# Performance work log

Measured on AMD Instinct MI355X. Metric: run time of the kernel, lower is better.

The kernel has to match this reference:

```python
import jax, jax.numpy as jnp
import numpy as np

D = 256      # input_dim
H = 8        # n_heads
HD = D // H  # head_dim = 32
B = 8
S = 127      # seq_len (feature tokens)
N = S + 1    # new_seq (CLS + features)
LN_EPS = 1e-5


def setup_inputs() -> dict:
    key = jax.random.key(0)
    ks = jax.random.split(key, 20)
    g = 0.02
    inp = {
        "desc_embeddings": jax.random.normal(ks[0], (B, S, D), jnp.float32),
        "name_value_embeddings": jax.random.normal(ks[1], (B, N, D), jnp.float32),
        # q/k/v projections (stored [in, out])
        "wq": jax.random.normal(ks[2], (D, D), jnp.float32) * g,
        "bq": jnp.zeros((D,), jnp.float32),
        "wk": jax.random.normal(ks[3], (D, D), jnp.float32) * g,
        "bk": jnp.zeros((D,), jnp.float32),
        "wv": jax.random.normal(ks[4], (D, D), jnp.float32) * g,
        "bv": jnp.zeros((D,), jnp.float32),
        # edge_update: Linear(2D->D), LayerNorm(D), ReLU, Linear(D->D)
        "ew1": jax.random.normal(ks[5], (2 * D, D), jnp.float32) * g,
        "eb1": jnp.zeros((D,), jnp.float32),
        "ln_g": jnp.ones((D,), jnp.float32),
        "ln_b": jnp.zeros((D,), jnp.float32),
        "ew2": jax.random.normal(ks[6], (D, D), jnp.float32) * g,
        "eb2": jnp.zeros((D,), jnp.float32),
        # attn_proj: Linear(3*head_dim -> 1)
        "attn_w": jax.random.normal(ks[7], (3 * HD,), jnp.float32) * g,
        "attn_b": jnp.zeros((), jnp.float32),
        # out_proj
        "wo": jax.random.normal(ks[8], (D, D), jnp.float32) * g,
        "bo": jnp.zeros((D,), jnp.float32),
    }
    return inp


def _forward(desc, nv, wq, bq, wk, bk, wv, bv, ew1, eb1, ln_g, ln_b, ew2, eb2,
             attn_w, attn_b, wo, bo):
    b, n, d = nv.shape
    s = n - 1
    # new adjacency: [1:,1:] = ones minus diag; row 0 (CLS->var) = 1; col 0 = 0; [0,0]=0
    adj = jnp.zeros((n, n), nv.dtype)
    adj = adj.at[1:, 1:].set(1.0 - jnp.eye(s, dtype=nv.dtype))
    adj = adj.at[0, 1:].set(1.0)
    adj = jnp.broadcast_to(adj, (b, n, n))  # [B,N,N]

    # edge attributes: var-var pairs concat(desc_i, desc_j); CLS row/col concat(desc_j, desc_j)
    var_edge = jnp.concatenate([
        jnp.broadcast_to(desc[:, :, None, :], (b, s, s, d)),
        jnp.broadcast_to(desc[:, None, :, :], (b, s, s, d)),
    ], axis=-1)                                   # [B,S,S,2D]
    cls_edge = jnp.concatenate([desc, desc], -1)  # [B,S,2D]
    ea = jnp.zeros((b, n, n, 2 * d), nv.dtype)
    ea = ea.at[:, 1:, 1:, :].set(var_edge)
    ea = ea.at[:, 0, 1:, :].set(cls_edge)
    ea = ea.at[:, 1:, 0, :].set(cls_edge)

    # edge MLP: Linear -> LayerNorm -> ReLU -> Linear
    h = ea @ ew1 + eb1                            # [B,N,N,D]
    mu = jnp.mean(h, -1, keepdims=True)
    var = jnp.mean((h - mu) ** 2, -1, keepdims=True)
    h = (h - mu) * jax.lax.rsqrt(var + LN_EPS) * ln_g + ln_b
    h = jax.nn.relu(h)
    e = h @ ew2 + eb2                             # [B,N,N,D]
    e = e.reshape(b, n, n, H, HD).transpose(0, 3, 1, 2, 4)  # [B,H,N,N,hd]
    e = e * adj[:, None, :, :, None]

    def heads(x, w, bias):
        return (x @ w + bias).reshape(b, n, H, HD).transpose(0, 2, 1, 3)  # [B,H,N,hd]

    q = heads(nv, wq, bq)
    k = heads(nv, wk, bk)
    v = heads(nv, wv, bv)

    # attn_proj(cat(q_i, k_j, e_ij)) decomposes additively over the three chunks
    w_q, w_k, w_e = attn_w[:HD], attn_w[HD:2 * HD], attn_w[2 * HD:]
    aq = jnp.einsum('bhid,d->bhi', q, w_q)
    ak = jnp.einsum('bhjd,d->bhj', k, w_k)
    ae = jnp.einsum('bhijd,d->bhij', e, w_e)
    scores = aq[:, :, :, None] + ak[:, :, None, :] + ae + attn_b  # [B,H,N,N]
    scores = scores + (adj[:, None] == 0).astype(scores.dtype) * (-1e9)
    attn = jax.nn.softmax(scores, axis=-1)

    ctx = jnp.einsum('bhij,bhjd->bhid', attn, v)                  # [B,H,N,hd]
    ctx = ctx.transpose(0, 2, 1, 3).reshape(b, n, d)
    out = ctx @ wo + bo
    return out, attn


def reference(desc_embeddings, name_value_embeddings, wq, bq, wk, bk, wv, bv,
              ew1, eb1, ln_g, ln_b, ew2, eb2, attn_w, attn_b, wo, bo):
    return _forward(desc_embeddings, name_value_embeddings, wq, bq, wk, bk, wv, bv,
                    ew1, eb1, ln_g, ln_b, ew2, eb2, attn_w, attn_b, wo, bo)
```

## Files before the change

kernel.cpp:

```cpp
#include <hip/hip_runtime.h>
#include <math.h>

namespace {
constexpr int D = 256;
constexpr int H = 8;
constexpr int HD = 32;
constexpr int B = 8;
constexpr int S = 127;
constexpr int N = 128;
constexpr float LN_EPS = 1e-5f;

constexpr int WS_P1T = 0;
constexpr int WS_P2T = WS_P1T + B * D * N;
constexpr int WS_V   = WS_P2T + B * D * N;
constexpr int WS_AQ  = WS_V + B * N * D;
constexpr int WS_AK  = WS_AQ + B * H * N;
constexpr int WS_FQK = WS_AK + B * H * N;
constexpr int WS_V2  = WS_FQK + D * 16;
constexpr int WS_BF  = WS_V2 + D * H;
constexpr int WS_ST  = WS_BF + 32;
constexpr int WS_RSTD = WS_ST + B * 512;
constexpr int WS_MB   = WS_RSTD + B * N * N;

typedef float f32x2 __attribute__((ext_vector_type(2)));
union F4 { float4 v; f32x2 h[2]; float f[4]; };
}

__global__ __launch_bounds__(256) void k1_fold(
    const float* __restrict__ wq, const float* __restrict__ wk,
    const float* __restrict__ ew2, const float* __restrict__ bq,
    const float* __restrict__ bk, const float* __restrict__ eb2,
    const float* __restrict__ attn_w, float* __restrict__ ws) {
  float* FQK = ws + WS_FQK;
  float* V2T = ws + WS_V2;
  float* BF  = ws + WS_BF;
  const int tg = blockIdx.x * 256 + threadIdx.x;
  if (tg < 6144) {
    const int mat = tg >> 11;
    const int rem = tg & 2047;
    const int c = rem >> 3;
    const int h = rem & 7;
    const float* W = (mat == 0) ? wq : (mat == 1) ? wk : ew2;
    const float* aw = attn_w + mat * HD;
    const float* wrow = W + c * D + h * HD;
    float s = 0.f;
#pragma unroll
    for (int d = 0; d < HD; ++d) s = fmaf(wrow[d], aw[d], s);
    if (mat < 2) FQK[c * 16 + mat * 8 + h] = s;
    else         V2T[h * D + c] = s;
  } else if (tg < 6168) {
    const int idx = tg - 6144;
    const int mat = idx >> 3;
    const int h = idx & 7;
    const float* bias = (mat == 0) ? bq : (mat == 1) ? bk : eb2;
    const float* aw = attn_w + mat * HD;
    float s = 0.f;
#pragma unroll
    for (int d = 0; d < HD; ++d) s = fmaf(bias[h * HD + d], aw[d], s);
    BF[mat * 8 + h] = s;
  }
}

__global__ __launch_bounds__(256) void kA_pre(
    const float* __restrict__ desc, const float* __restrict__ ew1,
    const float* __restrict__ eb1,
    const float* __restrict__ nv, const float* __restrict__ wv,
    const float* __restrict__ bv, float* __restrict__ ws) {
  const int blk = blockIdx.x;
  const int t = threadIdx.x;
  __shared__ float rows[4][264];
  __shared__ float fqks[D * 16];
  __shared__ float aqred2[2][64];

  if (blk < 256) {
    float* P1Tf = ws + WS_P1T;
    float* P2Tf = ws + WS_P2T;
    const int b = blk >> 5;
    const int i0 = (blk & 31) * 4;
    {
      const int r = t >> 6, c4 = t & 63;
      const int row = i0 + r;
      F4 dv;
      if (row < S) dv.v = *(const float4*)&desc[(b * S + row) * D + c4 * 4];
      else         dv.v = make_float4(0.f, 0.f, 0.f, 0.f);
      *(float4*)&rows[r][c4 * 4] = dv.v;
    }
    __syncthreads();
    const int o4 = t & 63;
    const int grp = t >> 6;
    const int m = grp >> 1;
    const int rp = grp & 1;
    const float* W = ew1 + m * D * D;
    F4 a0, a1;
    a0.v = make_float4(0.f, 0.f, 0.f, 0.f);
    a1.v = make_float4(0.f, 0.f, 0.f, 0.f);
    for (int c2 = 0; c2 < D; ++c2) {
      F4 w; w.v = *(const float4*)&W[c2 * D + o4 * 4];
      const float s0 = rows[rp * 2][c2];
      const float s1 = rows[rp * 2 + 1][c2];
#pragma unroll
      for (int e = 0; e < 4; ++e) {
        a0.f[e] = fmaf(s0, w.f[e], a0.f[e]);
        a1.f[e] = fmaf(s1, w.f[e], a1.f[e]);
      }
    }
    F4 ebv;
    if (m == 0) ebv.v = *(const float4*)&eb1[o4 * 4];
    else        ebv.v = make_float4(0.f, 0.f, 0.f, 0.f);
    F4 o0, o1;
#pragma unroll
    for (int e = 0; e < 4; ++e) {
      o0.f[e] = a0.f[e] + ebv.f[e];
      o1.f[e] = a1.f[e] + ebv.f[e];
    }
    float* PT = (m == 0) ? P1Tf : P2Tf;
    const int rbase = (b * 64 + o4) * 512;
    const int row0i = i0 + rp * 2;
    const int row1i = row0i + 1;
    if (row0i < S) *(float4*)&PT[rbase + row0i * 4] = o0.v;
    if (row1i < S) *(float4*)&PT[rbase + row1i * 4] = o1.v;
    float sv0 = 0.f, qv0 = 0.f, sv1 = 0.f, qv1 = 0.f;
#pragma unroll
    for (int e = 0; e < 4; ++e) {
      sv0 += o0.f[e]; qv0 = fmaf(o0.f[e], o0.f[e], qv0);
      sv1 += o1.f[e]; qv1 = fmaf(o1.f[e], o1.f[e], qv1);
    }
#pragma unroll
    for (int o = 1; o < 64; o <<= 1) {
      sv0 += __shfl_xor(sv0, o);
      qv0 += __shfl_xor(qv0, o);
      sv1 += __shfl_xor(sv1, o);
      qv1 += __shfl_xor(qv1, o);
    }
    if (o4 == 0) {
      float* STW = ws + WS_ST + b * 512 + m * 256;
      if (row0i < S) { STW[row0i] = sv0; STW[128 + row0i] = qv0; }
      if (row1i < S) { STW[row1i] = sv1; STW[128 + row1i] = qv1; }
    }
  } else {
    float* Vf  = ws + WS_V;
    float* AQ  = ws + WS_AQ;
    float* AK  = ws + WS_AK;
    const float* FQK = ws + WS_FQK;
    const float* BF  = ws + WS_BF;
    const int blk2 = blk - 256;
    const int b = blk2 >> 5;
    const int j0 = (blk2 & 31) * 4;
    {
      const int r = t >> 6, c4 = t & 63;
      *(float4*)&rows[r][c4 * 4] =
          *(const float4*)&nv[(b * N + j0 + r) * D + c4 * 4];
      float4* fq4 = (float4*)fqks;
      const float4* FQK4 = (const float4*)FQK;
#pragma unroll
      for (int k = 0; k < 4; ++k) fq4[k * 256 + t] = FQK4[k * 256 + t];
    }
    __syncthreads();
    if (t < 64) {
      const int o4 = t;
      F4 acc[4];
#pragma unroll
      for (int r = 0; r < 4; ++r) acc[r].v = make_float4(0.f, 0.f, 0.f, 0.f);
      for (int c2 = 0; c2 < D; ++c2) {
        F4 w; w.v = *(const float4*)&wv[c2 * D + o4 * 4];
#pragma unroll
        for (int r = 0; r < 4; ++r) {
          const float s = rows[r][c2];
#pragma unroll
          for (int e = 0; e < 4; ++e)
            acc[r].f[e] = fmaf(s, w.f[e], acc[r].f[e]);
        }
      }
      F4 b4; b4.v = *(const float4*)&bv[o4 * 4];
#pragma unroll
      for (int r = 0; r < 4; ++r) {
#pragma unroll
        for (int e = 0; e < 4; ++e) acc[r].f[e] += b4.f[e];
        *(float4*)&Vf[(b * N + j0 + r) * D + o4 * 4] = acc[r].v;
      }
    } else if (t < 192) {
      const int idx = t - 64;
      const int il = idx >> 5;
      const int oi = idx & 15;
      const int ch = (idx >> 4) & 1;
      float s = 0.f;
      for (int c = ch * 128; c < ch * 128 + 128; ++c)
        s = fmaf(rows[il][c], fqks[c * 16 + oi], s);
      aqred2[ch][il * 16 + oi] = s;
    }
    __syncthreads();
    if (t < 64) {
      const int il = t >> 4, oi = t & 15;
      const float s2 = aqred2[0][t] + aqred2[1][t] + BF[oi];
      if (oi < 8) AQ[(b * H + oi) * N + j0 + il] = s2;
      else        AK[(b * H + (oi - 8)) * N + j0 + il] = s2;
    }
  }
}

__global__ __launch_bounds__(512) void kG_stats(float* __restrict__ ws) {
  const int bid = blockIdx.x;
  const int wg = (bid & 7) * 32 + (bid >> 3);
  const int b = wg >> 5;
  const int ip0 = (wg & 31) * 4;
  const int t = threadIdx.x;
  const int jp = t & 127;
  const int cg = t >> 7;

  __shared__ float p1t[1024];
  __shared__ float gred[4][4][128];

  const float* P1Tf = ws + WS_P1T;
  const float4* P24 = reinterpret_cast<const float4*>(ws + WS_P2T);
  const float* ST = ws + WS_ST + b * 512;
  float* RST = ws + WS_RSTD + b * N * N;
  float* MBP = ws + WS_MB + b * N * N;
  const int base4 = b * 64 * 128;

  for (int k = t; k < 1024; k += 512) {
    const int r = k >> 8, c = k & 255;
    const int row = ip0 + r;
    p1t[r * 256 + c] = (row < S)
        ? P1Tf[(b * 64 + (c >> 2)) * 512 + row * 4 + (c & 3)] : 0.f;
  }
  F4 pp[16];
#pragma unroll
  for (int cc = 0; cc < 16; ++cc)
    pp[cc].v = P24[base4 + (cg * 16 + cc) * 128 + jp];
  __syncthreads();

  float g[4] = {0.f, 0.f, 0.f, 0.f};
#pragma unroll
  for (int cc = 0; cc < 16; ++cc) {
    const int c4 = cg * 16 + cc;
#pragma unroll
    for (int r = 0; r < 4; ++r) {
      F4 p1; p1.v = *(const float4*)&p1t[r * 256 + c4 * 4];
      g[r] = fmaf(pp[cc].f[0], p1.f[0], g[r]);
      g[r] = fmaf(pp[cc].f[1], p1.f[1], g[r]);
      g[r] = fmaf(pp[cc].f[2], p1.f[2], g[r]);
      g[r] = fmaf(pp[cc].f[3], p1.f[3], g[r]);
    }
  }
#pragma unroll
  for (int r = 0; r < 4; ++r) gred[cg][r][jp] = g[r];
  __syncthreads();
  {
    const int r2 = t >> 7, jp2 = t & 127;
    const float G = gred[0][r2][jp2] + gred[1][r2][jp2]
                  + gred[2][r2][jp2] + gred[3][r2][jp2];
    const int ip = ip0 + r2;
    const float S1 = ST[0 * 128 + ip], Q1 = ST[1 * 128 + ip];
    const float S2 = ST[2 * 128 + jp2], Q2 = ST[3 * 128 + jp2];
    const float mean = (S1 + S2) * (1.f / 256.f);
    const float var = (Q1 + Q2 + 2.f * G) * (1.f / 256.f) - mean * mean;
    const float rstd = 1.f / sqrtf(var + LN_EPS);
    RST[ip * N + jp2] = rstd;
    MBP[ip * N + jp2] = -mean * rstd;
  }
}

__global__ __launch_bounds__(512) void k4_attn(
    const float* __restrict__ ws,
    const float* __restrict__ ln_g, const float* __restrict__ ln_b,
    const float* __restrict__ attn_bp, float* __restrict__ attnp) {
  const int bid = blockIdx.x;
  const int wg = (bid & 7) * 64 + (bid >> 3);
  const int b = wg >> 6;
  const int i0 = (wg & 63) * 2;
  const int t = threadIdx.x;
  const int jl = t & 127;
  const int cq = t >> 7;

  __shared__ float v2s[H * D];
  __shared__ float gbs[2 * D];
  __shared__ float p1e[2][D];
  __shared__ float dsh[4][128][9];
  __shared__ float aqs[2][8];
  __shared__ float redm[8][2], reds[8][2];

  const float* P1Tf = ws + WS_P1T;
  const float* AQ   = ws + WS_AQ;
  const float* AK   = ws + WS_AK;
  const float* BF   = ws + WS_BF;
  const float* v2p  = ws + WS_V2;
  const float* RST  = ws + WS_RSTD + b * N * N;
  const float* MBP  = ws + WS_MB + b * N * N;

  reinterpret_cast<float4*>(v2s)[t] = reinterpret_cast<const float4*>(v2p)[t];
  if (t < 256) { gbs[t] = ln_g[t]; gbs[256 + t] = ln_b[t]; }
  {
    const int r = t >> 8, c = t & 255;
    const int row = i0 + r - 1;
    p1e[r][c] = (row >= 0)
        ? P1Tf[(b * 64 + (c >> 2)) * 512 + row * 4 + (c & 3)] : 0.f;
  }
  if (t < 16) {
    const int r = t >> 3, h = t & 7;
    aqs[r][h] = AQ[(b * H + h) * N + i0 + r] + BF[16 + h] + attn_bp[0];
  }

  const int jm1 = (jl == 0) ? 0 : jl - 1;
  const bool blk0 = (i0 == 0);
  f32x2 rstd2[2], mb2[2];
#pragma unroll
  for (int r = 0; r < 2; ++r) {
    const int irow = i0 + r;
    const int ip = (irow == 0) ? jm1 : (irow - 1);
    const float rs = RST[ip * N + jm1];
    const float mb = MBP[ip * N + jm1];
    rstd2[r].x = rs; rstd2[r].y = rs;
    mb2[r].x = mb; mb2[r].y = mb;
  }
  float akr[2];
#pragma unroll
  for (int hh = 0; hh < 2; ++hh)
    akr[hh] = AK[(b * H + cq * 2 + hh) * N + jl];
  const f32x2 zero2 = {0.f, 0.f};
  __syncthreads();

  const float4* P14 = reinterpret_cast<const float4*>(ws + WS_P1T);
  const float4* P24 = reinterpret_cast<const float4*>(ws + WS_P2T);
  const int base4 = b * 64 * 128;
  const int c4lo = cq * 16;

  f32x2 dt2[2][8];
#pragma unroll
  for (int r = 0; r < 2; ++r)
#pragma unroll
    for (int h = 0; h < 8; ++h) dt2[r][h] = zero2;
  F4 p2c;
  p2c.v = P24[base4 + c4lo * 128 + jm1];
  for (int cc = 0; cc < 16; ++cc) {
    const int c4 = c4lo + cc;
    F4 p2 = p2c;
    if (cc < 15) p2c.v = P24[base4 + (c4 + 1) * 128 + jm1];
    F4 g4; g4.v = *(const float4*)&gbs[c4 * 4];
    F4 b4; b4.v = *(const float4*)&gbs[256 + c4 * 4];
    F4 p1r[2];
    if (blk0) p1r[0].v = P14[base4 + c4 * 128 + jm1];
    else      p1r[0].v = *(const float4*)&p1e[0][c4 * 4];
    p1r[1].v = *(const float4*)&p1e[1][c4 * 4];
    f32x2 w2[2][2];
#pragma unroll
    for (int r = 0; r < 2; ++r) {
#pragma unroll
      for (int pp = 0; pp < 2; ++pp) {
        const f32x2 u2 = p1r[r].h[pp] + p2.h[pp];
        const f32x2 zt2 = __builtin_elementwise_fma(u2, rstd2[r], mb2[r]);
        const f32x2 z2 = __builtin_elementwise_fma(zt2, g4.h[pp], b4.h[pp]);
        w2[r][pp] = __builtin_elementwise_max(z2, zero2);
      }
    }
#pragma unroll
    for (int h = 0; h < 8; ++h) {
      F4 v2v; v2v.v = *(const float4*)&v2s[h * D + c4 * 4];
      dt2[0][h] = __builtin_elementwise_fma(w2[0][0], v2v.h[0], dt2[0][h]);
      dt2[0][h] = __builtin_elementwise_fma(w2[0][1], v2v.h[1], dt2[0][h]);
      dt2[1][h] = __builtin_elementwise_fma(w2[1][0], v2v.h[0], dt2[1][h]);
      dt2[1][h] = __builtin_elementwise_fma(w2[1][1], v2v.h[1], dt2[1][h]);
    }
  }

  const int w = t >> 6;
  for (int r = 0; r < 2; ++r) {
#pragma unroll
    for (int h = 0; h < 8; ++h) dsh[cq][jl][h] = dt2[r][h].x + dt2[r][h].y;
    __syncthreads();
    const int irow = i0 + r;
    const bool masked = (jl == 0) || (jl == irow);
    float sc[2], pr[2];
#pragma unroll
    for (int hh = 0; hh < 2; ++hh) {
      const int h = cq * 2 + hh;
      const float dsum = dsh[0][jl][h] + dsh[1][jl][h]
                       + dsh[2][jl][h] + dsh[3][jl][h];
      const float v = aqs[r][h] + akr[hh] + dsum;
      sc[hh] = masked ? -INFINITY : v;
    }
    float mx[2];
#pragma unroll
    for (int hh = 0; hh < 2; ++hh) {
      float v = sc[hh];
#pragma unroll
      for (int o = 1; o < 64; o <<= 1) v = fmaxf(v, __shfl_xor(v, o));
      mx[hh] = v;
    }
    if ((t & 63) == 0) { redm[w][0] = mx[0]; redm[w][1] = mx[1]; }
    __syncthreads();
#pragma unroll
    for (int hh = 0; hh < 2; ++hh) {
      const float m = fmaxf(redm[w][hh], redm[w ^ 1][hh]);
      pr[hh] = expf(sc[hh] - m);
    }
    float sm[2];
#pragma unroll
    for (int hh = 0; hh < 2; ++hh) {
      float v = pr[hh];
#pragma unroll
      for (int o = 1; o < 64; o <<= 1) v += __shfl_xor(v, o);
      sm[hh] = v;
    }
    if ((t & 63) == 0) { reds[w][0] = sm[0]; reds[w][1] = sm[1]; }
    __syncthreads();
#pragma unroll
    for (int hh = 0; hh < 2; ++hh) {
      const int h = cq * 2 + hh;
      const float at = pr[hh] / (reds[w][hh] + reds[w ^ 1][hh]);
      attnp[((b * H + h) * N + irow) * N + jl] = at;
    }
    __syncthreads();
  }
}

__global__ __launch_bounds__(512) void k5_out(
    const float* __restrict__ ws, const float* __restrict__ attnp,
    const float* __restrict__ wo, const float* __restrict__ bo,
    float* __restrict__ outp) {
  const int bid = blockIdx.x;
  const int wg = (bid & 7) * 32 + (bid >> 3);
  const int b = wg >> 5;
  const int i0 = (wg & 31) * 4;
  const int t = threadIdx.x;
  const int o4 = t & 63;
  const int grp = t >> 6;

  __shared__ float attn_sh[4][H][136];
  __shared__ float red[4][8][64][4];
  __shared__ float ctxs[4][260];

#pragma unroll
  for (int k = 0; k < 2; ++k) {
    const int idx = k * 512 + t;
    const int r = idx >> 8, h = (idx >> 5) & 7, j4 = idx & 31;
    const float4 a =
        *(const float4*)&attnp[((b * H + h) * N + i0 + r) * N + j4 * 4];
    *(float4*)&attn_sh[r][h][j4 * 4] = a;
  }
  __syncthreads();

  const int hh = o4 >> 3;
  const float* Vb = ws + WS_V + b * N * D;
  F4 acc[4];
#pragma unroll
  for (int r = 0; r < 4; ++r) acc[r].v = make_float4(0.f, 0.f, 0.f, 0.f);
  for (int jj = 0; jj < 16; ++jj) {
    const int j = grp * 16 + jj;
    F4 v4; v4.v = *(const float4*)&Vb[j * D + o4 * 4];
#pragma unroll
    for (int r = 0; r < 4; ++r) {
      const float a = attn_sh[r][hh][j];
#pragma unroll
      for (int e = 0; e < 4; ++e) acc[r].f[e] = fmaf(a, v4.f[e], acc[r].f[e]);
    }
  }
#pragma unroll
  for (int r = 0; r < 4; ++r) *(float4*)&red[r][grp][o4][0] = acc[r].v;
  __syncthreads();
  if (t < 256) {
    const int oc = t & 63, r = t >> 6;
    F4 s; s.v = make_float4(0.f, 0.f, 0.f, 0.f);
#pragma unroll
    for (int g = 0; g < 8; ++g) {
      F4 p; p.v = *(const float4*)&red[r][g][oc][0];
#pragma unroll
      for (int e = 0; e < 4; ++e) s.f[e] += p.f[e];
    }
    *(float4*)&ctxs[r][oc * 4] = s.v;
  }
  __syncthreads();

  F4 acc2[4];
#pragma unroll
  for (int r = 0; r < 4; ++r) acc2[r].v = make_float4(0.f, 0.f, 0.f, 0.f);
  for (int cc = 0; cc < 32; ++cc) {
    const int c2 = grp * 32 + cc;
    F4 w4; w4.v = *(const float4*)&wo[c2 * D + o4 * 4];
#pragma unroll
    for (int r = 0; r < 4; ++r) {
      const float cx = ctxs[r][c2];
#pragma unroll
      for (int e = 0; e < 4; ++e)
        acc2[r].f[e] = fmaf(cx, w4.f[e], acc2[r].f[e]);
    }
  }
#pragma unroll
  for (int r = 0; r < 4; ++r) *(float4*)&red[r][grp][o4][0] = acc2[r].v;
  __syncthreads();
  if (t < 256) {
    const int oc = t & 63, r = t >> 6;
    F4 s; s.v = *(const float4*)&bo[oc * 4];
#pragma unroll
    for (int g = 0; g < 8; ++g) {
      F4 p; p.v = *(const float4*)&red[r][g][oc][0];
#pragma unroll
      for (int e = 0; e < 4; ++e) s.f[e] += p.f[e];
    }
    *(float4*)&outp[(b * N + i0 + r) * D + oc * 4] = s.v;
  }
}

extern "C" void kernel_launch(void* const* d_in, const int* in_sizes, int n_in,
                              void* d_out, int out_size, void* d_ws, size_t ws_size,
                              hipStream_t stream) {
  (void)in_sizes; (void)n_in; (void)out_size; (void)ws_size;
  const float* desc = (const float*)d_in[0];
  const float* nv   = (const float*)d_in[1];
  const float* wq   = (const float*)d_in[2];
  const float* bq   = (const float*)d_in[3];
  const float* wk   = (const float*)d_in[4];
  const float* bk   = (const float*)d_in[5];
  const float* wv   = (const float*)d_in[6];
  const float* bv   = (const float*)d_in[7];
  const float* ew1  = (const float*)d_in[8];
  const float* eb1  = (const float*)d_in[9];
  const float* ln_g = (const float*)d_in[10];
  const float* ln_b = (const float*)d_in[11];
  const float* ew2  = (const float*)d_in[12];
  const float* eb2  = (const float*)d_in[13];
  const float* aw   = (const float*)d_in[14];
  const float* ab   = (const float*)d_in[15];
  const float* wo   = (const float*)d_in[16];
  const float* bo   = (const float*)d_in[17];

  float* ws   = (float*)d_ws;
  float* outp = (float*)d_out;
  float* attnp = outp + B * N * D;

  k1_fold<<<25, 256, 0, stream>>>(wq, wk, ew2, bq, bk, eb2, aw, ws);
  kA_pre<<<512, 256, 0, stream>>>(desc, ew1, eb1, nv, wv, bv, ws);
  kG_stats<<<256, 512, 0, stream>>>(ws);
  k4_attn<<<B * 64, 512, 0, stream>>>(ws, ln_g, ln_b, ab, attnp);
  k5_out<<<256, 512, 0, stream>>>(ws, attnp, wo, bo, outp);
}
```

Baseline: 52.61 us.

## Widen row tiles in pre-projection and attention kernels, split-K with LDS reduction

kA_pre now runs 512-thread blocks that each handle 8 rows instead of 4. The K dimension is split across four thread groups and the partial sums are combined through a shared-memory reduction, so each weight load is reused across more rows. k4_attn now processes 4 query rows per block instead of 2, which halves the block count and reuses each P2 load and v2s read across twice as many rows. This adds register pressure (dt2[4][8], acc[8]) and shared memory, and it lowers the number of blocks, which may hurt occupancy and latency hiding.

```diff
diff --git a/kernel.cpp b/kernel.cpp
--- a/kernel.cpp
+++ b/kernel.cpp
@@ -61,22 +61,23 @@
   }
 }
 
-__global__ __launch_bounds__(256) void kA_pre(
+__global__ __launch_bounds__(512) void kA_pre(
     const float* __restrict__ desc, const float* __restrict__ ew1,
     const float* __restrict__ eb1,
     const float* __restrict__ nv, const float* __restrict__ wv,
     const float* __restrict__ bv, float* __restrict__ ws) {
   const int blk = blockIdx.x;
   const int t = threadIdx.x;
-  __shared__ float rows[4][264];
+  __shared__ float rows[8][264];
+  __shared__ float red[8][4][64][4];
   __shared__ float fqks[D * 16];
-  __shared__ float aqred2[2][64];
-
-  if (blk < 256) {
+  __shared__ float aqred2[2][128];
+
+  if (blk < 128) {
     float* P1Tf = ws + WS_P1T;
     float* P2Tf = ws + WS_P2T;
-    const int b = blk >> 5;
-    const int i0 = (blk & 31) * 4;
+    const int b = blk >> 4;
+    const int i0 = (blk & 15) * 8;
     {
       const int r = t >> 6, c4 = t & 63;
       const int row = i0 + r;
@@ -88,98 +89,103 @@
     __syncthreads();
     const int o4 = t & 63;
     const int grp = t >> 6;
-    const int m = grp >> 1;
-    const int rp = grp & 1;
+    const int m = grp >> 2;
+    const int q = grp & 3;
     const float* W = ew1 + m * D * D;
-    F4 a0, a1;
-    a0.v = make_float4(0.f, 0.f, 0.f, 0.f);
-    a1.v = make_float4(0.f, 0.f, 0.f, 0.f);
-    for (int c2 = 0; c2 < D; ++c2) {
+    F4 acc[8];
+#pragma unroll
+    for (int r = 0; r < 8; ++r) acc[r].v = make_float4(0.f, 0.f, 0.f, 0.f);
+    for (int cc = 0; cc < 64; ++cc) {
+      const int c2 = q * 64 + cc;
       F4 w; w.v = *(const float4*)&W[c2 * D + o4 * 4];
-      const float s0 = rows[rp * 2][c2];
-      const float s1 = rows[rp * 2 + 1][c2];
-#pragma unroll
-      for (int e = 0; e < 4; ++e) {
-        a0.f[e] = fmaf(s0, w.f[e], a0.f[e]);
-        a1.f[e] = fmaf(s1, w.f[e], a1.f[e]);
-      }
-    }
-    F4 ebv;
-    if (m == 0) ebv.v = *(const float4*)&eb1[o4 * 4];
-    else        ebv.v = make_float4(0.f, 0.f, 0.f, 0.f);
-    F4 o0, o1;
-#pragma unroll
-    for (int e = 0; e < 4; ++e) {
-      o0.f[e] = a0.f[e] + ebv.f[e];
-      o1.f[e] = a1.f[e] + ebv.f[e];
-    }
-    float* PT = (m == 0) ? P1Tf : P2Tf;
-    const int rbase = (b * 64 + o4) * 512;
-    const int row0i = i0 + rp * 2;
-    const int row1i = row0i + 1;
-    if (row0i < S) *(float4*)&PT[rbase + row0i * 4] = o0.v;
-    if (row1i < S) *(float4*)&PT[rbase + row1i * 4] = o1.v;
-    float sv0 = 0.f, qv0 = 0.f, sv1 = 0.f, qv1 = 0.f;
-#pragma unroll
-    for (int e = 0; e < 4; ++e) {
-      sv0 += o0.f[e]; qv0 = fmaf(o0.f[e], o0.f[e], qv0);
-      sv1 += o1.f[e]; qv1 = fmaf(o1.f[e], o1.f[e], qv1);
-    }
-#pragma unroll
-    for (int o = 1; o < 64; o <<= 1) {
-      sv0 += __shfl_xor(sv0, o);
-      qv0 += __shfl_xor(qv0, o);
-      sv1 += __shfl_xor(sv1, o);
-      qv1 += __shfl_xor(qv1, o);
-    }
-    if (o4 == 0) {
-      float* STW = ws + WS_ST + b * 512 + m * 256;
-      if (row0i < S) { STW[row0i] = sv0; STW[128 + row0i] = qv0; }
-      if (row1i < S) { STW[row1i] = sv1; STW[128 + row1i] = qv1; }
+#pragma unroll
+      for (int r = 0; r < 8; ++r) {
+        const float s = rows[r][c2];
+#pragma unroll
+        for (int e = 0; e < 4; ++e) acc[r].f[e] = fmaf(s, w.f[e], acc[r].f[e]);
+      }
+    }
+#pragma unroll
+    for (int mm = 0; mm < 2; ++mm) {
+      if (m == mm) {
+#pragma unroll
+        for (int r = 0; r < 8; ++r) *(float4*)&red[r][q][o4][0] = acc[r].v;
+      }
+      __syncthreads();
+      {
+        const int r = t >> 6;
+        F4 s; s.v = make_float4(0.f, 0.f, 0.f, 0.f);
+#pragma unroll
+        for (int g = 0; g < 4; ++g) {
+          F4 p; p.v = *(const float4*)&red[r][g][o4][0];
+#pragma unroll
+          for (int e = 0; e < 4; ++e) s.f[e] += p.f[e];
+        }
+        if (mm == 0) {
+          F4 eb; eb.v = *(const float4*)&eb1[o4 * 4];
+#pragma unroll
+          for (int e = 0; e < 4; ++e) s.f[e] += eb.f[e];
+        }
+        const int row = i0 + r;
+        float* PT = (mm == 0) ? P1Tf : P2Tf;
+        if (row < S) *(float4*)&PT[(b * 64 + o4) * 512 + row * 4] = s.v;
+        float sv = 0.f, qv = 0.f;
+#pragma unroll
+        for (int e = 0; e < 4; ++e) {
+          sv += s.f[e];
+          qv = fmaf(s.f[e], s.f[e], qv);
+        }
+#pragma unroll
+        for (int o = 1; o < 64; o <<= 1) {
+          sv += __shfl_xor(sv, o);
+          qv += __shfl_xor(qv, o);
+        }
+        if (o4 == 0 && row < S) {
+          float* STW = ws + WS_ST + b * 512 + mm * 256;
+          STW[row] = sv;
+          STW[128 + row] = qv;
+        }
+      }
+      __syncthreads();
     }
   } else {
     float* Vf  = ws + WS_V;
     float* AQ  = ws + WS_AQ;
     float* AK  = ws + WS_AK;
-    const float* FQK = ws + WS_FQK;
-    const float* BF  = ws + WS_BF;
-    const int blk2 = blk - 256;
-    const int b = blk2 >> 5;
-    const int j0 = (blk2 & 31) * 4;
+    const float* BF = ws + WS_BF;
+    const int blk2 = blk - 128;
+    const int b = blk2 >> 4;
+    const int j0 = (blk2 & 15) * 8;
     {
       const int r = t >> 6, c4 = t & 63;
       *(float4*)&rows[r][c4 * 4] =
           *(const float4*)&nv[(b * N + j0 + r) * D + c4 * 4];
       float4* fq4 = (float4*)fqks;
-      const float4* FQK4 = (const float4*)FQK;
-#pragma unroll
-      for (int k = 0; k < 4; ++k) fq4[k * 256 + t] = FQK4[k * 256 + t];
-    }
-    __syncthreads();
-    if (t < 64) {
-      const int o4 = t;
-      F4 acc[4];
-#pragma unroll
-      for (int r = 0; r < 4; ++r) acc[r].v = make_float4(0.f, 0.f, 0.f, 0.f);
-      for (int c2 = 0; c2 < D; ++c2) {
+      const float4* FQK4 = (const float4*)(ws + WS_FQK);
+      fq4[t] = FQK4[t];
+      fq4[512 + t] = FQK4[512 + t];
+    }
+    __syncthreads();
+    if (t < 256) {
+      const int o4 = t & 63, q = t >> 6;
+      F4 acc[8];
+#pragma unroll
+      for (int r = 0; r < 8; ++r) acc[r].v = make_float4(0.f, 0.f, 0.f, 0.f);
+      for (int cc = 0; cc < 64; ++cc) {
+        const int c2 = q * 64 + cc;
         F4 w; w.v = *(const float4*)&wv[c2 * D + o4 * 4];
 #pragma unroll
-        for (int r = 0; r < 4; ++r) {
+        for (int r = 0; r < 8; ++r) {
           const float s = rows[r][c2];
 #pragma unroll
           for (int e = 0; e < 4; ++e)
             acc[r].f[e] = fmaf(s, w.f[e], acc[r].f[e]);
         }
       }
-      F4 b4; b4.v = *(const float4*)&bv[o4 * 4];
-#pragma unroll
-      for (int r = 0; r < 4; ++r) {
-#pragma unroll
-        for (int e = 0; e < 4; ++e) acc[r].f[e] += b4.f[e];
-        *(float4*)&Vf[(b * N + j0 + r) * D + o4 * 4] = acc[r].v;
-      }
-    } else if (t < 192) {
-      const int idx = t - 64;
+#pragma unroll
+      for (int r = 0; r < 8; ++r) *(float4*)&red[r][q][o4][0] = acc[r].v;
+    } else {
+      const int idx = t - 256;
       const int il = idx >> 5;
       const int oi = idx & 15;
       const int ch = (idx >> 4) & 1;
@@ -189,7 +195,21 @@
       aqred2[ch][il * 16 + oi] = s;
     }
     __syncthreads();
-    if (t < 64) {
+    {
+      const int r = t >> 6, o4 = t & 63;
+      F4 s; s.v = make_float4(0.f, 0.f, 0.f, 0.f);
+#pragma unroll
+      for (int g = 0; g < 4; ++g) {
+        F4 p; p.v = *(const float4*)&red[r][g][o4][0];
+#pragma unroll
+        for (int e = 0; e < 4; ++e) s.f[e] += p.f[e];
+      }
+      F4 b4; b4.v = *(const float4*)&bv[o4 * 4];
+#pragma unroll
+      for (int e = 0; e < 4; ++e) s.f[e] += b4.f[e];
+      *(float4*)&Vf[(b * N + j0 + r) * D + o4 * 4] = s.v;
+    }
+    if (t < 128) {
       const int il = t >> 4, oi = t & 15;
       const float s2 = aqred2[0][t] + aqred2[1][t] + BF[oi];
       if (oi < 8) AQ[(b * H + oi) * N + j0 + il] = s2;
@@ -265,18 +285,18 @@
     const float* __restrict__ ln_g, const float* __restrict__ ln_b,
     const float* __restrict__ attn_bp, float* __restrict__ attnp) {
   const int bid = blockIdx.x;
-  const int wg = (bid & 7) * 64 + (bid >> 3);
-  const int b = wg >> 6;
-  const int i0 = (wg & 63) * 2;
+  const int wg = (bid & 7) * 32 + (bid >> 3);
+  const int b = wg >> 5;
+  const int i0 = (wg & 31) * 4;
   const int t = threadIdx.x;
   const int jl = t & 127;
   const int cq = t >> 7;
 
   __shared__ float v2s[H * D];
   __shared__ float gbs[2 * D];
-  __shared__ float p1e[2][D];
+  __shared__ float p1e[4][D];
   __shared__ float dsh[4][128][9];
-  __shared__ float aqs[2][8];
+  __shared__ float aqs[4][8];
   __shared__ float redm[8][2], reds[8][2];
 
   const float* P1Tf = ws + WS_P1T;
@@ -289,22 +309,22 @@
 
   reinterpret_cast<float4*>(v2s)[t] = reinterpret_cast<const float4*>(v2p)[t];
   if (t < 256) { gbs[t] = ln_g[t]; gbs[256 + t] = ln_b[t]; }
-  {
-    const int r = t >> 8, c = t & 255;
+  for (int k = t; k < 4 * D; k += 512) {
+    const int r = k >> 8, c = k & 255;
     const int row = i0 + r - 1;
     p1e[r][c] = (row >= 0)
         ? P1Tf[(b * 64 + (c >> 2)) * 512 + row * 4 + (c & 3)] : 0.f;
   }
-  if (t < 16) {
+  if (t < 32) {
     const int r = t >> 3, h = t & 7;
     aqs[r][h] = AQ[(b * H + h) * N + i0 + r] + BF[16 + h] + attn_bp[0];
   }
 
   const int jm1 = (jl == 0) ? 0 : jl - 1;
   const bool blk0 = (i0 == 0);
-  f32x2 rstd2[2], mb2[2];
-#pragma unroll
-  for (int r = 0; r < 2; ++r) {
+  f32x2 rstd2[4], mb2[4];
+#pragma unroll
+  for (int r = 0; r < 4; ++r) {
     const int irow = i0 + r;
     const int ip = (irow == 0) ? jm1 : (irow - 1);
     const float rs = RST[ip * N + jm1];
@@ -324,9 +344,9 @@
   const int base4 = b * 64 * 128;
   const int c4lo = cq * 16;
 
-  f32x2 dt2[2][8];
-#pragma unroll
-  for (int r = 0; r < 2; ++r)
+  f32x2 dt2[4][8];
+#pragma unroll
+  for (int r = 0; r < 4; ++r)
 #pragma unroll
     for (int h = 0; h < 8; ++h) dt2[r][h] = zero2;
   F4 p2c;
@@ -337,13 +357,15 @@
     if (cc < 15) p2c.v = P24[base4 + (c4 + 1) * 128 + jm1];
     F4 g4; g4.v = *(const float4*)&gbs[c4 * 4];
     F4 b4; b4.v = *(const float4*)&gbs[256 + c4 * 4];
-    F4 p1r[2];
+    F4 p1r[4];
     if (blk0) p1r[0].v = P14[base4 + c4 * 128 + jm1];
     else      p1r[0].v = *(const float4*)&p1e[0][c4 * 4];
     p1r[1].v = *(const float4*)&p1e[1][c4 * 4];
-    f32x2 w2[2][2];
-#pragma unroll
-    for (int r = 0; r < 2; ++r) {
+    p1r[2].v = *(const float4*)&p1e[2][c4 * 4];
+    p1r[3].v = *(const float4*)&p1e[3][c4 * 4];
+    f32x2 w2[4][2];
+#pragma unroll
+    for (int r = 0; r < 4; ++r) {
 #pragma unroll
       for (int pp = 0; pp < 2; ++pp) {
         const f32x2 u2 = p1r[r].h[pp] + p2.h[pp];
@@ -355,15 +377,16 @@
 #pragma unroll
     for (int h = 0; h < 8; ++h) {
       F4 v2v; v2v.v = *(const float4*)&v2s[h * D + c4 * 4];
-      dt2[0][h] = __builtin_elementwise_fma(w2[0][0], v2v.h[0], dt2[0][h]);
-      dt2[0][h] = __builtin_elementwise_fma(w2[0][1], v2v.h[1], dt2[0][h]);
-      dt2[1][h] = __builtin_elementwise_fma(w2[1][0], v2v.h[0], dt2[1][h]);
-      dt2[1][h] = __builtin_elementwise_fma(w2[1][1], v2v.h[1], dt2[1][h]);
+#pragma unroll
+      for (int r = 0; r < 4; ++r) {
+        dt2[r][h] = __builtin_elementwise_fma(w2[r][0], v2v.h[0], dt2[r][h]);
+        dt2[r][h] = __builtin_elementwise_fma(w2[r][1], v2v.h[1], dt2[r][h]);
+      }
     }
   }
 
   const int w = t >> 6;
-  for (int r = 0; r < 2; ++r) {
+  for (int r = 0; r < 4; ++r) {
 #pragma unroll
     for (int h = 0; h < 8; ++h) dsh[cq][jl][h] = dt2[r][h].x + dt2[r][h].y;
     __syncthreads();
@@ -528,8 +551,8 @@
   float* attnp = outp + B * N * D;
 
   k1_fold<<<25, 256, 0, stream>>>(wq, wk, ew2, bq, bk, eb2, aw, ws);
-  kA_pre<<<512, 256, 0, stream>>>(desc, ew1, eb1, nv, wv, bv, ws);
+  kA_pre<<<256, 512, 0, stream>>>(desc, ew1, eb1, nv, wv, bv, ws);
   kG_stats<<<256, 512, 0, stream>>>(ws);
-  k4_attn<<<B * 64, 512, 0, stream>>>(ws, ln_g, ln_b, ab, attnp);
+  k4_attn<<<B * 32, 512, 0, stream>>>(ws, ln_g, ln_b, ab, attnp);
   k5_out<<<256, 512, 0, stream>>>(ws, attnp, wo, bo, outp);
 }
```

Result: faster. 46.91 us, median of 2 (-10.8%).
